# Optimization experiments

Hardware: AMD Instinct MI355X
Metric: run time of the kernel (lower is better)

## Reference

```python
import jax, jax.numpy as jnp
import numpy as np

B, S, C, H = 2, 2048, 1280, 20
D = C // H  # head_dim = 64


def setup_inputs() -> dict:
    key = jax.random.key(0)
    ks = jax.random.split(key, 5)
    scale = 1.0 / np.sqrt(C)
    return {
        "hidden_states": jax.random.normal(ks[0], (B, S, C), dtype=jnp.float32),
        "Wq": jax.random.normal(ks[1], (C, C), dtype=jnp.float32) * scale,
        "Wk": jax.random.normal(ks[2], (C, C), dtype=jnp.float32) * scale,
        "Wv": jax.random.normal(ks[3], (C, C), dtype=jnp.float32) * scale,
        "Wo": jax.random.normal(ks[4], (C, C), dtype=jnp.float32) * scale,
        "bo": jnp.zeros((C,), dtype=jnp.float32),
    }


def reference(hidden_states, Wq, Wk, Wv, Wo, bo):
    residual = hidden_states
    # q/k/v projections (self-attention: encoder_hidden_states is None)
    q = hidden_states @ Wq  # [B,S,C]
    k = hidden_states @ Wk
    v = hidden_states @ Wv
    # split heads -> [B,H,S,D]
    q = q.reshape(B, S, H, D).transpose(0, 2, 1, 3)
    k = k.reshape(B, S, H, D).transpose(0, 2, 1, 3)
    v = v.reshape(B, S, H, D).transpose(0, 2, 1, 3)
    scale = 1.0 / np.sqrt(D)
    scores = jnp.einsum('bhqd,bhkd->bhqk', q, k) * scale  # [B,H,S,S]
    attn_probs = jax.nn.softmax(scores, axis=-1)
    # loss term: Frobenius norm of the full attention-prob tensor (fp32)
    loss = jnp.sqrt(jnp.sum(jnp.square(attn_probs.astype(jnp.float32))))
    out = jnp.einsum('bhqk,bhkd->bhqd', attn_probs, v)  # [B,H,S,D]
    out = out.transpose(0, 2, 1, 3).reshape(B, S, C)
    out = out @ Wo + bo
    out = out + residual  # residual_connection=True, rescale_output_factor=1.0
    return out, loss
```

## Files before the change

### kernel.cpp

```cpp
#include <hip/hip_runtime.h>
#include <hip/hip_bf16.h>
#include <math.h>

#define B_SZ   2
#define S_LEN  2048
#define C_DIM  1280
#define H_NUM  20
#define D_HEAD 64
#define M_TOT  (B_SZ * S_LEN)

typedef __bf16 bf16;
typedef __bf16 bf16x8 __attribute__((ext_vector_type(8)));
typedef __bf16 bf16x4 __attribute__((ext_vector_type(4)));
typedef float  f32x4  __attribute__((ext_vector_type(4)));

__device__ inline f32x4 zero4() { f32x4 z; z[0]=z[1]=z[2]=z[3]=0.f; return z; }

__device__ __forceinline__ void async_copy16(void* lds, const void* g) {
    __builtin_amdgcn_global_load_lds(
        (const __attribute__((address_space(1))) unsigned int*)g,
        (__attribute__((address_space(3))) unsigned int*)lds,
        16, 0, 0);
}

__global__ __launch_bounds__(256) void k_convert_hs(const float* __restrict__ in,
                                                    bf16* __restrict__ out) {
    int i = (blockIdx.x * 256 + threadIdx.x) * 4;
    float4 v = *(const float4*)(in + i);
    bf16x4 o; o[0]=(bf16)v.x; o[1]=(bf16)v.y; o[2]=(bf16)v.z; o[3]=(bf16)v.w;
    *(bf16x4*)(out + i) = o;
}

__global__ __launch_bounds__(256) void k_transpose_w(
    const float* __restrict__ w0, const float* __restrict__ w1,
    const float* __restrict__ w2, const float* __restrict__ w3,
    bf16* __restrict__ o0, bf16* __restrict__ o1,
    bf16* __restrict__ o2, bf16* __restrict__ o3) {
    __shared__ float t[32][33];
    const float* w = blockIdx.z==0 ? w0 : blockIdx.z==1 ? w1 : blockIdx.z==2 ? w2 : w3;
    bf16*       o  = blockIdx.z==0 ? o0 : blockIdx.z==1 ? o1 : blockIdx.z==2 ? o2 : o3;
    int k0 = blockIdx.y*32, n0 = blockIdx.x*32;
    int tx = threadIdx.x & 31, ty = threadIdx.x >> 5;
    #pragma unroll
    for (int i = 0; i < 32; i += 8)
        t[ty+i][tx] = w[(size_t)(k0+ty+i)*C_DIM + n0 + tx];
    __syncthreads();
    #pragma unroll
    for (int i = 0; i < 32; i += 8)
        o[(size_t)(n0+ty+i)*C_DIM + k0 + tx] = (bf16)t[tx][ty+i];
}

#define QBM 256
#define QBN 256
#define QBK 32
#define QNT (C_DIM / QBK)
__global__ __launch_bounds__(512, 2) void k_gemm_qkv(
    const bf16* __restrict__ A,
    const bf16* __restrict__ Wcat,
    bf16* __restrict__ Qo, bf16* __restrict__ Ko, bf16* __restrict__ VTo) {
    __shared__ bf16 lds[3][2][QBM][QBK];
    const int m0  = blockIdx.y * QBM;
    const int nx  = blockIdx.x;
    const int z   = nx / 5;
    const int nw0 = (nx % 5) * QBN;
    const int ng0 = nx * QBN;
    const int tid = threadIdx.x, lane = tid & 63, wid = tid >> 6;
    const int wm = wid >> 2, wn = wid & 3;
    const int g = lane >> 4, lr = lane & 15;
    const float scale = (z==0) ? 0.18033688011112042f : 1.0f;

    f32x4 acc[8][4];
    #pragma unroll
    for (int i=0;i<8;i++)
        #pragma unroll
        for (int j=0;j<4;j++)
            acc[i][j] = zero4();

#define QSTAGE(bf, kt)                                                       \
    { const int k0_ = (kt)*QBK;                                              \
      _Pragma("unroll")                                                      \
      for (int c = 0; c < 2; ++c) {                                          \
        int p = c*512 + tid;                                                 \
        int row = p >> 2, gp = p & 3;                                        \
        async_copy16((char*)&lds[bf][0][0][0] + p*16,                        \
                     &A[(size_t)(m0+row)*C_DIM + k0_ + gp*8]);               \
        async_copy16((char*)&lds[bf][1][0][0] + p*16,                        \
                     &Wcat[(size_t)(ng0+row)*C_DIM + k0_ + gp*8]);           \
      } }

    QSTAGE(0, 0);
    QSTAGE(1, 1);
    asm volatile("s_waitcnt vmcnt(4)" ::: "memory");
    __builtin_amdgcn_s_barrier();

    int cur = 0;
    for (int t = 0; t < QNT; ++t) {
        if (t + 2 < QNT) {
            int sb = cur + 2; if (sb >= 3) sb -= 3;
            QSTAGE(sb, t + 2);
        }
        const bf16* AB = &lds[cur][0][0][0];
        const bf16* BB = &lds[cur][1][0][0];
        bf16x8 af[8], bfr[4];
        #pragma unroll
        for (int mf = 0; mf < 8; ++mf)
            af[mf] = *(const bf16x8*)(AB + (wm*128 + mf*16 + lr)*QBK + g*8);
        #pragma unroll
        for (int nf = 0; nf < 4; ++nf)
            bfr[nf] = *(const bf16x8*)(BB + (wn*64 + nf*16 + lr)*QBK + g*8);
        #pragma unroll
        for (int mf = 0; mf < 8; ++mf)
            #pragma unroll
            for (int nf = 0; nf < 4; ++nf)
                acc[mf][nf] = __builtin_amdgcn_mfma_f32_16x16x32_bf16(
                    af[mf], bfr[nf], acc[mf][nf], 0,0,0);
        if (t + 2 < QNT) asm volatile("s_waitcnt vmcnt(4) lgkmcnt(0)" ::: "memory");
        else             asm volatile("s_waitcnt vmcnt(0) lgkmcnt(0)" ::: "memory");
        __builtin_amdgcn_s_barrier();
        if (++cur == 3) cur = 0;
    }

    if (z == 2) {
        #pragma unroll
        for (int mf=0;mf<8;mf++) {
            #pragma unroll
            for (int nf=0;nf<4;nf++) {
                int n = nw0 + wn*64 + nf*16 + lr;
                int h = n >> 6, d = n & 63;
                int m = m0 + wm*128 + mf*16 + g*4;
                int b = m >> 11, s = m & (S_LEN-1);
                bf16x4 ov;
                #pragma unroll
                for (int r=0;r<4;r++) ov[r] = (bf16)acc[mf][nf][r];
                *(bf16x4*)&VTo[((size_t)(b*H_NUM + h)*D_HEAD + d)*S_LEN + s] = ov;
            }
        }
    } else {
        bf16* Out = (z==0) ? Qo : Ko;
        #pragma unroll
        for (int mf=0;mf<8;mf++) {
            #pragma unroll
            for (int nf=0;nf<4;nf++) {
                int n = nw0 + wn*64 + nf*16 + lr;
                int h = n >> 6, d = n & 63;
                #pragma unroll
                for (int r=0;r<4;r++) {
                    int m = m0 + wm*128 + mf*16 + g*4 + r;
                    int b = m >> 11, s = m & (S_LEN-1);
                    Out[(size_t)((b*H_NUM + h)*S_LEN + s)*D_HEAD + d] = (bf16)(acc[mf][nf][r] * scale);
                }
            }
        }
    }
}

#define BM 128
#define BN 128
#define BK 64

#define GEMM_STAGE(Al, Bl, Aptr, Bptr, m0, n0, k0)                                \
    {                                                                             \
        _Pragma("unroll")                                                         \
        for (int c = 0; c < 4; ++c) {                                             \
            int p = c*256 + tid;                                                  \
            int row = p >> 3, gp = p & 7, gc = gp ^ (row & 7);                    \
            async_copy16((char*)(Al) + p*16,                                      \
                         &Aptr[(size_t)((m0)+row)*C_DIM + (k0) + gc*8]);          \
            async_copy16((char*)(Bl) + p*16,                                      \
                         &Bptr[(size_t)((n0)+row)*C_DIM + (k0) + gc*8]);          \
        }                                                                         \
    }

#define GEMM_COMPUTE(Al, Bl)                                                      \
    {                                                                             \
        _Pragma("unroll")                                                         \
        for (int kk = 0; kk < 2; ++kk) {                                          \
            bf16x8 af[4], bfr[4];                                                 \
            _Pragma("unroll")                                                     \
            for (int mf = 0; mf < 4; ++mf) {                                      \
                int arow = wm*64 + mf*16 + lr;                                    \
                af[mf] = *(const bf16x8*)((char*)(Al) + arow*128 +                \
                          (((kk*4 + g) ^ (arow & 7)) << 4));                      \
            }                                                                     \
            _Pragma("unroll")                                                     \
            for (int nf = 0; nf < 4; ++nf) {                                      \
                int brow = wn*64 + nf*16 + lr;                                    \
                bfr[nf] = *(const bf16x8*)((char*)(Bl) + brow*128 +               \
                          (((kk*4 + g) ^ (brow & 7)) << 4));                      \
            }                                                                     \
            _Pragma("unroll")                                                     \
            for (int mf = 0; mf < 4; ++mf)                                        \
                _Pragma("unroll")                                                 \
                for (int nf = 0; nf < 4; ++nf)                                    \
                    acc[mf][nf] = __builtin_amdgcn_mfma_f32_16x16x32_bf16(        \
                        af[mf], bfr[nf], acc[mf][nf], 0,0,0);                     \
        }                                                                         \
    }

__global__ __launch_bounds__(256) void k_gemm_out(
    const bf16* __restrict__ A,
    const bf16* __restrict__ WoT,
    const float* __restrict__ bo,
    const float* __restrict__ res,
    float* __restrict__ out) {
    __shared__ bf16 Al[2][BM][BK];
    __shared__ bf16 Bl[2][BN][BK];
    const int m0 = blockIdx.y * BM, n0 = blockIdx.x * BN;
    const int tid = threadIdx.x, lane = tid & 63, wid = tid >> 6;
    const int wm = wid >> 1, wn = wid & 1;
    const int g = lane >> 4, lr = lane & 15;
    f32x4 acc[4][4];
    #pragma unroll
    for (int i=0;i<4;i++)
        #pragma unroll
        for (int j=0;j<4;j++)
            acc[i][j] = zero4();
    GEMM_STAGE(&Al[0][0][0], &Bl[0][0][0], A, WoT, m0, n0, 0);
    asm volatile("s_waitcnt vmcnt(0)" ::: "memory");
    __builtin_amdgcn_s_barrier();
    int cur = 0;
    for (int k0 = 0; k0 < C_DIM; k0 += BK) {
        if (k0 + BK < C_DIM)
            GEMM_STAGE(&Al[cur^1][0][0], &Bl[cur^1][0][0], A, WoT, m0, n0, k0 + BK);
        GEMM_COMPUTE(&Al[cur][0][0], &Bl[cur][0][0]);
        asm volatile("s_waitcnt vmcnt(0) lgkmcnt(0)" ::: "memory");
        __builtin_amdgcn_s_barrier();
        cur ^= 1;
    }
    #pragma unroll
    for (int mf=0;mf<4;mf++) {
        #pragma unroll
        for (int nf=0;nf<4;nf++) {
            int n = n0 + wn*64 + nf*16 + lr;
            float bias = bo[n];
            #pragma unroll
            for (int r=0;r<4;r++) {
                int m = m0 + wm*64 + mf*16 + g*4 + r;
                size_t idx = (size_t)m*C_DIM + n;
                out[idx] = acc[mf][nf][r] + bias + res[idx];
            }
        }
    }
}

#define KVB 64
__global__ __launch_bounds__(256) void k_attn(
    const bf16* __restrict__ Q,
    const bf16* __restrict__ Kg,
    const bf16* __restrict__ VT,
    bf16* __restrict__ O,
    float* __restrict__ lossPart) {
    __shared__ bf16 Kl[2][KVB][64];
    __shared__ bf16 Vl[2][D_HEAD][64];

    const int id  = blockIdx.x;
    const int fid = (id & 7) * 160 + (id >> 3);
    const int bh = fid >> 5;
    const int qb = fid & 31;
    const int b = bh / H_NUM, hh = bh % H_NUM;
    const int tid = threadIdx.x, lane = tid & 63, wid = tid >> 6;
    const int g = lane >> 4, lr = lane & 15;

    const bf16* Kbase = Kg + (size_t)bh * S_LEN * D_HEAD;
    const bf16* Vbase = VT + (size_t)bh * D_HEAD * S_LEN;

    const int qrow = qb*64 + wid*16 + lr;
    const bf16* qp = Q + ((size_t)bh*S_LEN + qrow)*D_HEAD;
    const bf16x8 aq0 = *(const bf16x8*)(qp + g*8);
    const bf16x8 aq1 = *(const bf16x8*)(qp + 32 + g*8);

    bf16x8 ones;
    #pragma unroll
    for (int i=0;i<8;i++) ones[i] = (bf16)1.0f;

    const int lb7 = (lr & 3) | (((lr >> 2) & 1) << 2);
    const int lhi = ((lr >> 2) & 2) << 3;

    f32x4 o_acc[4];
    #pragma unroll
    for (int i=0;i<4;i++) o_acc[i] = zero4();
    f32x4 l_acc = zero4();
    f32x4 s2m   = zero4();

#define STAGE(buf, kv0)                                                          \
    {                                                                            \
        _Pragma("unroll")                                                        \
        for (int pp=0; pp<2; ++pp) {                                             \
            int p = pp*256 + tid;                                                \
            int lrow = p >> 3, gp = p & 7;                                       \
            int tl = (lrow & 51) | ((lrow & 4) << 1) | ((lrow & 8) >> 1);        \
            async_copy16((char*)&Kl[buf][0][0] + p*16,                           \
                         Kbase + (size_t)((kv0) + tl)*D_HEAD                     \
                               + ((gp ^ (lrow & 7)) << 3));                      \
        }                                                                        \
        _Pragma("unroll")                                                        \
        for (int pp=0; pp<2; ++pp) {                                             \
            int p = pp*256 + tid;                                                \
            int drow = p >> 3, gp = p & 7;                                       \
            async_copy16((char*)&Vl[buf][0][0] + p*16,                           \
                         Vbase + (size_t)drow*S_LEN + (kv0)                      \
                               + ((gp ^ (drow & 7)) << 3));                      \
        }                                                                        \
    }

    STAGE(0, 0);
    __syncthreads();

    for (int t = 0; t < S_LEN/KVB; ++t) {
        const int cur = t & 1;
        if (t + 1 < S_LEN/KVB) STAGE(cur^1, (t+1)*KVB);
        const bf16* KB = &Kl[cur][0][0];
        const bf16* VB = &Vl[cur][0][0];

        f32x4 accp[2][2];
        __builtin_amdgcn_s_setprio(1);
        #pragma unroll
        for (int pair=0; pair<2; ++pair)
            #pragma unroll
            for (int u=0; u<2; ++u) {
                const bf16* kr = KB + (pair*32 + (u<<3) + lhi + lb7)*64;
                bf16x8 k0 = *(const bf16x8*)(kr + ((g       ^ lb7) << 3));
                bf16x8 k1 = *(const bf16x8*)(kr + (((4 + g) ^ lb7) << 3));
                f32x4 c = zero4();
                c = __builtin_amdgcn_mfma_f32_16x16x32_bf16(k0, aq0, c, 0,0,0);
                c = __builtin_amdgcn_mfma_f32_16x16x32_bf16(k1, aq1, c, 0,0,0);
                accp[pair][u] = c;
            }
        __builtin_amdgcn_s_setprio(0);
        bf16x8 pb[2];
        #pragma unroll
        for (int pair=0; pair<2; ++pair)
            #pragma unroll
            for (int u=0; u<2; ++u)
                #pragma unroll
                for (int r=0; r<4; ++r) {
                    float e = __builtin_amdgcn_exp2f(accp[pair][u][r]);
                    pb[pair][u*4+r] = (bf16)e;
                }
        __builtin_amdgcn_s_setprio(1);
        l_acc = __builtin_amdgcn_mfma_f32_16x16x32_bf16(ones, pb[0], l_acc, 0,0,0);
        l_acc = __builtin_amdgcn_mfma_f32_16x16x32_bf16(ones, pb[1], l_acc, 0,0,0);
        s2m = __builtin_amdgcn_mfma_f32_16x16x32_bf16(pb[0], pb[0], s2m, 0,0,0);
        s2m = __builtin_amdgcn_mfma_f32_16x16x32_bf16(pb[1], pb[1], s2m, 0,0,0);
        #pragma unroll
        for (int ds_=0; ds_<4; ++ds_) {
            const bf16* vr = VB + (ds_*16 + lr)*64;
            #pragma unroll
            for (int pair=0; pair<2; ++pair) {
                bf16x8 v = *(const bf16x8*)(vr + (((pair*4 + g) ^ (lr & 7)) << 3));
                o_acc[ds_] = __builtin_amdgcn_mfma_f32_16x16x32_bf16(v, pb[pair], o_acc[ds_], 0,0,0);
            }
        }
        __builtin_amdgcn_s_setprio(0);
        __syncthreads();
    }

    const float lfull = l_acc[0];

    const float inv = 1.0f / lfull;
    bf16* orow = O + ((size_t)(b*S_LEN + qrow)*H_NUM + hh)*D_HEAD;
    #pragma unroll
    for (int ds_=0; ds_<4; ++ds_) {
        bf16x4 ov;
        #pragma unroll
        for (int r=0; r<4; ++r) ov[r] = (bf16)(o_acc[ds_][r] * inv);
        *(bf16x4*)(orow + ds_*16 + g*4) = ov;
    }
    float v = 0.f;
    if (g == (lr >> 2)) v = s2m[lr & 3] / (lfull * lfull);
    #pragma unroll
    for (int msk=1; msk<64; msk<<=1) v += __shfl_xor(v, msk);
    if (lane == 0) lossPart[(bh*32 + qb)*4 + wid] = v;
}

__global__ __launch_bounds__(256) void k_loss(const float* __restrict__ part,
                                              float* __restrict__ out, int n) {
    __shared__ float w[4];
    float s = 0.f;
    for (int i = threadIdx.x; i < n; i += 256) s += part[i];
    #pragma unroll
    for (int msk=1; msk<64; msk<<=1) s += __shfl_xor(s, msk);
    int lane = threadIdx.x & 63, wid = threadIdx.x >> 6;
    if (lane==0) w[wid] = s;
    __syncthreads();
    if (threadIdx.x==0) out[(size_t)M_TOT*C_DIM] = sqrtf(w[0]+w[1]+w[2]+w[3]);
}

extern "C" void kernel_launch(void* const* d_in, const int* in_sizes, int n_in,
                              void* d_out, int out_size, void* d_ws, size_t ws_size,
                              hipStream_t stream) {
    (void)in_sizes; (void)n_in; (void)out_size; (void)ws_size;
    const float* hs = (const float*)d_in[0];
    const float* Wq = (const float*)d_in[1];
    const float* Wk = (const float*)d_in[2];
    const float* Wv = (const float*)d_in[3];
    const float* Wo = (const float*)d_in[4];
    const float* bo = (const float*)d_in[5];
    float* out = (float*)d_out;

    constexpr size_t HS_E = (size_t)M_TOT * C_DIM;
    constexpr size_t W_E  = (size_t)C_DIM * C_DIM;
    char* ws = (char*)d_ws;
    size_t off = 0;
    bf16* hs_bf = (bf16*)(ws + off); off += HS_E * 2;
    bf16* WqT   = (bf16*)(ws + off); off += W_E * 2;
    bf16* WkT   = (bf16*)(ws + off); off += W_E * 2;
    bf16* WvT   = (bf16*)(ws + off); off += W_E * 2;
    bf16* WoT   = (bf16*)(ws + off); off += W_E * 2;
    bf16* Qb    = (bf16*)(ws + off); off += HS_E * 2;
    bf16* Kb    = (bf16*)(ws + off); off += HS_E * 2;
    bf16* Vtb   = (bf16*)(ws + off); off += HS_E * 2;
    bf16* Ob    = (bf16*)(ws + off); off += HS_E * 2;
    float* lossPart = (float*)(ws + off); off += 5120 * 4;

    k_convert_hs<<<HS_E/(256*4), 256, 0, stream>>>(hs, hs_bf);
    k_transpose_w<<<dim3(C_DIM/32, C_DIM/32, 4), 256, 0, stream>>>(Wq, Wk, Wv, Wo, WqT, WkT, WvT, WoT);
    k_gemm_qkv<<<dim3(3*C_DIM/QBN, M_TOT/QBM), 512, 0, stream>>>(hs_bf, WqT, Qb, Kb, Vtb);
    k_attn<<<1280, 256, 0, stream>>>(Qb, Kb, Vtb, Ob, lossPart);
    k_gemm_out<<<dim3(C_DIM/BN, M_TOT/BM), 256, 0, stream>>>(Ob, WoT, bo, hs, out);
    k_loss<<<1, 256, 0, stream>>>(lossPart, out, 5120);
}
```

Before: 172.9 us.

## Merge prep kernels and double attention query tile to 128 rows

The bf16 conversion of hidden_states and the weight transposes are fused into one launch, with a flat block index split between the two tasks. The attention kernel now runs 512 threads (8 waves) per block covering 128 query rows, so each staged K/V tile in LDS serves twice as many queries. Each thread issues one async copy per tile instead of two, and the grid is halved with matching loss-partial indexing. This cuts K/V global traffic and one launch, but halves the block count (640 blocks), which may lower latency hiding on the GPU.

```diff
diff --git a/kernel.cpp b/kernel.cpp
--- a/kernel.cpp
+++ b/kernel.cpp
@@ -23,23 +23,26 @@
         16, 0, 0);
 }
 
-__global__ __launch_bounds__(256) void k_convert_hs(const float* __restrict__ in,
-                                                    bf16* __restrict__ out) {
-    int i = (blockIdx.x * 256 + threadIdx.x) * 4;
-    float4 v = *(const float4*)(in + i);
-    bf16x4 o; o[0]=(bf16)v.x; o[1]=(bf16)v.y; o[2]=(bf16)v.z; o[3]=(bf16)v.w;
-    *(bf16x4*)(out + i) = o;
-}
-
-__global__ __launch_bounds__(256) void k_transpose_w(
+__global__ __launch_bounds__(256) void k_prep(
+    const float* __restrict__ hs, bf16* __restrict__ hs_bf,
     const float* __restrict__ w0, const float* __restrict__ w1,
     const float* __restrict__ w2, const float* __restrict__ w3,
     bf16* __restrict__ o0, bf16* __restrict__ o1,
     bf16* __restrict__ o2, bf16* __restrict__ o3) {
+    if (blockIdx.x < 5120) {
+        int i = (blockIdx.x * 256 + threadIdx.x) * 4;
+        float4 v = *(const float4*)(hs + i);
+        bf16x4 o; o[0]=(bf16)v.x; o[1]=(bf16)v.y; o[2]=(bf16)v.z; o[3]=(bf16)v.w;
+        *(bf16x4*)(hs_bf + i) = o;
+        return;
+    }
     __shared__ float t[32][33];
-    const float* w = blockIdx.z==0 ? w0 : blockIdx.z==1 ? w1 : blockIdx.z==2 ? w2 : w3;
-    bf16*       o  = blockIdx.z==0 ? o0 : blockIdx.z==1 ? o1 : blockIdx.z==2 ? o2 : o3;
-    int k0 = blockIdx.y*32, n0 = blockIdx.x*32;
+    int idx = blockIdx.x - 5120;
+    int zi  = idx / 1600;
+    int rem = idx % 1600;
+    int k0 = (rem / 40) * 32, n0 = (rem % 40) * 32;
+    const float* w = zi==0 ? w0 : zi==1 ? w1 : zi==2 ? w2 : w3;
+    bf16*       o  = zi==0 ? o0 : zi==1 ? o1 : zi==2 ? o2 : o3;
     int tx = threadIdx.x & 31, ty = threadIdx.x >> 5;
     #pragma unroll
     for (int i = 0; i < 32; i += 8)
@@ -244,7 +247,7 @@
 }
 
 #define KVB 64
-__global__ __launch_bounds__(256) void k_attn(
+__global__ __launch_bounds__(512) void k_attn(
     const bf16* __restrict__ Q,
     const bf16* __restrict__ Kg,
     const bf16* __restrict__ VT,
@@ -254,9 +257,9 @@
     __shared__ bf16 Vl[2][D_HEAD][64];
 
     const int id  = blockIdx.x;
-    const int fid = (id & 7) * 160 + (id >> 3);
-    const int bh = fid >> 5;
-    const int qb = fid & 31;
+    const int fid = (id & 7) * 80 + (id >> 3);
+    const int bh = fid >> 4;
+    const int qb = fid & 15;
     const int b = bh / H_NUM, hh = bh % H_NUM;
     const int tid = threadIdx.x, lane = tid & 63, wid = tid >> 6;
     const int g = lane >> 4, lr = lane & 15;
@@ -264,7 +267,7 @@
     const bf16* Kbase = Kg + (size_t)bh * S_LEN * D_HEAD;
     const bf16* Vbase = VT + (size_t)bh * D_HEAD * S_LEN;
 
-    const int qrow = qb*64 + wid*16 + lr;
+    const int qrow = qb*128 + wid*16 + lr;
     const bf16* qp = Q + ((size_t)bh*S_LEN + qrow)*D_HEAD;
     const bf16x8 aq0 = *(const bf16x8*)(qp + g*8);
     const bf16x8 aq1 = *(const bf16x8*)(qp + 32 + g*8);
@@ -284,18 +287,16 @@
 
 #define STAGE(buf, kv0)                                                          \
     {                                                                            \
-        _Pragma("unroll")                                                        \
-        for (int pp=0; pp<2; ++pp) {                                             \
-            int p = pp*256 + tid;                                                \
+        {                                                                        \
+            int p = tid;                                                         \
             int lrow = p >> 3, gp = p & 7;                                       \
             int tl = (lrow & 51) | ((lrow & 4) << 1) | ((lrow & 8) >> 1);        \
             async_copy16((char*)&Kl[buf][0][0] + p*16,                           \
                          Kbase + (size_t)((kv0) + tl)*D_HEAD                     \
                                + ((gp ^ (lrow & 7)) << 3));                      \
         }                                                                        \
-        _Pragma("unroll")                                                        \
-        for (int pp=0; pp<2; ++pp) {                                             \
-            int p = pp*256 + tid;                                                \
+        {                                                                        \
+            int p = tid;                                                         \
             int drow = p >> 3, gp = p & 7;                                       \
             async_copy16((char*)&Vl[buf][0][0] + p*16,                           \
                          Vbase + (size_t)drow*S_LEN + (kv0)                      \
@@ -370,7 +371,7 @@
     if (g == (lr >> 2)) v = s2m[lr & 3] / (lfull * lfull);
     #pragma unroll
     for (int msk=1; msk<64; msk<<=1) v += __shfl_xor(v, msk);
-    if (lane == 0) lossPart[(bh*32 + qb)*4 + wid] = v;
+    if (lane == 0) lossPart[(bh*16 + qb)*8 + wid] = v;
 }
 
 __global__ __launch_bounds__(256) void k_loss(const float* __restrict__ part,
@@ -413,10 +414,9 @@
     bf16* Ob    = (bf16*)(ws + off); off += HS_E * 2;
     float* lossPart = (float*)(ws + off); off += 5120 * 4;
 
-    k_convert_hs<<<HS_E/(256*4), 256, 0, stream>>>(hs, hs_bf);
-    k_transpose_w<<<dim3(C_DIM/32, C_DIM/32, 4), 256, 0, stream>>>(Wq, Wk, Wv, Wo, WqT, WkT, WvT, WoT);
+    k_prep<<<11520, 256, 0, stream>>>(hs, hs_bf, Wq, Wk, Wv, Wo, WqT, WkT, WvT, WoT);
     k_gemm_qkv<<<dim3(3*C_DIM/QBN, M_TOT/QBM), 512, 0, stream>>>(hs_bf, WqT, Qb, Kb, Vtb);
-    k_attn<<<1280, 256, 0, stream>>>(Qb, Kb, Vtb, Ob, lossPart);
+    k_attn<<<640, 512, 0, stream>>>(Qb, Kb, Vtb, Ob, lossPart);
     k_gemm_out<<<dim3(C_DIM/BN, M_TOT/BM), 256, 0, stream>>>(Ob, WoT, bo, hs, out);
     k_loss<<<1, 256, 0, stream>>>(lossPart, out, 5120);
 }
```

Result: faster. 156.4 us (-9.6%).
